# Kernel tuning notes

Measured on AMD Instinct MI355X. Metric: run time of the kernel, lower is better.

## Reference

```python
import jax, jax.numpy as jnp
import numpy as np

MAX_SAMPLES = 400  # init max_samples
EPS = 1e-9


def setup_inputs() -> dict:
    key = jax.random.key(0)
    k1, k2, k3, k4 = jax.random.split(key, 4)
    E, N, K, L = 8192, 2048, 8, 16
    # per-edge probabilities (positive, as the loss takes log of ratios)
    probas = jax.random.uniform(k1, (E,), jnp.float32, minval=1e-3, maxval=1.0)
    # soft cluster assignments: row-normalized so Bhattacharyya coeff <= 1
    c = jax.random.uniform(k2, (N, K), jnp.float32)
    clusters = c / c.sum(axis=1, keepdims=True)
    edges_nn = jax.random.randint(k3, (E, 2), 0, N)
    label_keypoints = jax.random.randint(k4, (L,), 0, N)
    return {"probas": probas, "clusters": clusters,
            "edges_nn": edges_nn, "label_keypoints": label_keypoints}


def reference(probas, clusters, edges_nn, label_keypoints):
    E = edges_nn.shape[0]
    clst = jnp.argmax(clusters, axis=1)                      # [N] hard assignment
    c0 = clst[edges_nn[:, 0]]                                # [E]
    c1 = clst[edges_nn[:, 1]]                                # [E]
    assigned = clst[label_keypoints]                         # [L] clusters at keypoints
    # edge selected if either endpoint lies in a keypoint cluster (union over labels,
    # static-shape mask form of get_edges_on_location)
    sel = jnp.any((c0[None, :] == assigned[:, None]) |
                  (c1[None, :] == assigned[:, None]), axis=0)  # [E]
    sims = c0 == c1
    pos = sel & sims                                          # positive edges
    neg = sel & ~sims                                         # negative edges
    # Bhattacharyya coefficient per edge: sum_k sqrt(p_k * q_k)
    bc = jnp.sqrt(clusters[edges_nn[:, 0]] * clusters[edges_nn[:, 1]]).sum(axis=1)  # [E]
    # pos x neg cross product, restricted to pairs sharing the anchor node edges[.,0]
    same_anchor = edges_nn[:, 0][:, None] == edges_nn[None, :, 0]   # [E,E]
    valid = pos[:, None] & neg[None, :] & same_anchor               # [E,E]
    w = 1.0 - 0.5 * (bc[:, None] + bc[None, :])                     # [E,E] sampling prob
    logw = jnp.where(valid & (w > 0),
                     jnp.log(jnp.maximum(w, EPS)), -jnp.inf)
    # multinomial-without-replacement via Gumbel top-k (deterministic key)
    u = jax.random.uniform(jax.random.key(42), (E, E), jnp.float32)
    gumbel = -jnp.log(-jnp.log(u + EPS) + EPS)
    vals, flat_idx = jax.lax.top_k((logw + gumbel).reshape(-1), MAX_SAMPLES)
    i_ = flat_idx // E                                        # positive-edge rows
    j_ = flat_idx % E                                         # negative-edge rows
    p_pos = probas[i_]
    p_neg = probas[j_]
    term = jnp.log(p_pos / (p_pos + p_neg))                   # [max_samples]
    # guard against < max_samples valid pairs (torch would just sample fewer)
    ok = jnp.isfinite(vals)
    loss = -jnp.sum(jnp.where(ok, term, 0.0)) / jnp.maximum(jnp.sum(ok), 1)
    return loss
```

## Files before the change

kernel.cpp:

```cpp
#include <hip/hip_runtime.h>
#include <stdint.h>


#define E_CONST 8192
#define N_CONST 2048
#define K_CONST 8
#define L_CONST 16
#define MAXS 400
#define EPS_F 1e-9f
#define NTHR 1024

struct Cand { float val; uint32_t pack; };

__device__ __forceinline__ uint2 threefry2x32_42(uint32_t x0, uint32_t x1) {
    const uint32_t ks0 = 0u, ks1 = 42u;
    const uint32_t ks2 = ks0 ^ ks1 ^ 0x1BD11BDAu;
    const uint32_t ks[3] = {ks0, ks1, ks2};
    const int R[2][4] = {{13, 15, 26, 6}, {17, 29, 16, 24}};
    x0 += ks0; x1 += ks1;
#pragma unroll
    for (int g = 0; g < 5; ++g) {
        const int* r = R[g & 1];
#pragma unroll
        for (int q = 0; q < 4; ++q) {
            x0 += x1;
            x1 = (x1 << r[q]) | (x1 >> (32 - r[q]));
            x1 ^= x0;
        }
        x0 += ks[(g + 1) % 3];
        x1 += ks[(g + 2) % 3] + (uint32_t)(g + 1);
    }
    return make_uint2(x0, x1);
}

__device__ __forceinline__ float gumbel_at(uint32_t idx) {
    uint2 o = threefry2x32_42(0u, idx);
    uint32_t bits = o.x ^ o.y;
    float u = __uint_as_float((bits >> 9) | 0x3F800000u) - 1.0f;
    return -logf(-logf(u + EPS_F) + EPS_F);
}

__device__ __forceinline__ uint32_t sortable_key(float f) {
    uint32_t b = __float_as_uint(f);
    return (b & 0x80000000u) ? ~b : (b | 0x80000000u);
}

__device__ __forceinline__ int argmax8(float4 a, float4 b) {
    float v[8] = {a.x, a.y, a.z, a.w, b.x, b.y, b.z, b.w};
    float best = v[0]; int bi = 0;
#pragma unroll
    for (int k = 1; k < 8; ++k)
        if (v[k] > best) { best = v[k]; bi = k; }
    return bi;
}

__global__ __launch_bounds__(128) void k_prep(
    const float* __restrict__ clusters, const int* __restrict__ edges,
    const int* __restrict__ keypts,
    float* __restrict__ bc, unsigned char* __restrict__ flags) {
    __shared__ uint32_t s_mask;
    int tid = threadIdx.x;
    if (tid == 0) s_mask = 0;
    __syncthreads();
    if (tid < L_CONST) {
        const float4* r = (const float4*)(clusters + keypts[tid] * K_CONST);
        atomicOr(&s_mask, 1u << argmax8(r[0], r[1]));
    }
    __syncthreads();
    uint32_t m = s_mask;

    int e = blockIdx.x * 128 + tid;
    const int2* ed2 = (const int2*)edges;
    const float4* c4 = (const float4*)clusters;
    int2 p = ed2[e];
    float4 a0 = c4[2 * p.x], a1 = c4[2 * p.x + 1];
    float4 b0 = c4[2 * p.y], b1 = c4[2 * p.y + 1];
    int c0 = argmax8(a0, a1);
    int c1 = argmax8(b0, b1);
    float s = sqrtf(a0.x * b0.x);
    s += sqrtf(a0.y * b0.y);
    s += sqrtf(a0.z * b0.z);
    s += sqrtf(a0.w * b0.w);
    s += sqrtf(a1.x * b1.x);
    s += sqrtf(a1.y * b1.y);
    s += sqrtf(a1.z * b1.z);
    s += sqrtf(a1.w * b1.w);
    bc[e] = s;
    unsigned char f = 0;
    if ((((m >> c0) | (m >> c1)) & 1u)) f = (c0 == c1) ? 1 : 2;
    flags[e] = f;
}

__device__ __forceinline__ void scan_inplace(int* arr, int* tmp, int* totalOut) {
    int tid = threadIdx.x;
    int lane = tid & 63, wid = tid >> 6;
    int i0 = 2 * tid, i1 = i0 + 1;
    int v0 = arr[i0], v1 = arr[i1];
    int s = v0 + v1;
    int inc = s;
#pragma unroll
    for (int off = 1; off < 64; off <<= 1) {
        int u = __shfl_up(inc, off);
        if (lane >= off) inc += u;
    }
    if (lane == 63) tmp[wid] = inc;
    __syncthreads();
    if (wid == 0) {
        int w = (lane < 16) ? tmp[lane] : 0;
        int incw = w;
#pragma unroll
        for (int off = 1; off < 16; off <<= 1) {
            int u = __shfl_up(incw, off);
            if (lane >= off) incw += u;
        }
        if (lane < 16) tmp[lane] = incw - w;
    }
    __syncthreads();
    int base = tmp[wid] + (inc - s);
    arr[i0] = base;
    arr[i1] = base + v0;
    if (tid == 1023) *totalOut = base + v0 + v1;
    __syncthreads();
}

__global__ __launch_bounds__(1024) void k_fused(
    const float* __restrict__ probas, const int* __restrict__ edges,
    const unsigned char* __restrict__ flags, const float* __restrict__ bc,
    Cand* __restrict__ cand, int pmax, float* __restrict__ out) {

    __shared__ int s_pk[N_CONST];
    __shared__ int s_q[N_CONST];
    __shared__ int s_cur[N_CONST];
    __shared__ uint16_t s_csr[E_CONST];
    __shared__ int s_tmp[16];
    __shared__ int s_hist[256];
    __shared__ float s_wsum[16];
    __shared__ int s_wcnt[16];
    __shared__ int s_totPk, s_totQ;
    __shared__ uint32_t s_prefix;
    __shared__ int s_target;

    int tid = threadIdx.x;
    s_pk[2 * tid] = 0; s_pk[2 * tid + 1] = 0;
    __syncthreads();

    const int2* ed2 = (const int2*)edges;
    uint32_t af[8];
#pragma unroll
    for (int it = 0; it < 8; ++it) {
        int e = tid + it * NTHR;
        int a = ed2[e].x;
        int f = flags[e];
        af[it] = ((uint32_t)a << 2) | (uint32_t)f;
        if (f == 1)      atomicAdd(&s_pk[a], 1);
        else if (f == 2) atomicAdd(&s_pk[a], 0x10000);
    }
    __syncthreads();

    {
        int i0 = 2 * tid, i1 = i0 + 1;
        int p0 = s_pk[i0], p1 = s_pk[i1];
        s_q[i0] = (p0 & 0xFFFF) * (p0 >> 16);
        s_q[i1] = (p1 & 0xFFFF) * (p1 >> 16);
    }
    __syncthreads();
    scan_inplace(s_pk, s_tmp, &s_totPk);
    scan_inplace(s_q, s_tmp, &s_totQ);
    s_cur[2 * tid] = s_pk[2 * tid];
    s_cur[2 * tid + 1] = s_pk[2 * tid + 1];
    __syncthreads();
    int nPosTot = s_totPk & 0xFFFF;
    int nNegTot = s_totPk >> 16;
    int P = s_totQ; if (P > pmax) P = pmax;

#pragma unroll
    for (int it = 0; it < 8; ++it) {
        int f = (int)(af[it] & 3u);
        int a = (int)(af[it] >> 2);
        int e = tid + it * NTHR;
        if (f == 1) {
            int old = atomicAdd(&s_cur[a], 1);
            s_csr[old & 0xFFFF] = (uint16_t)e;
        } else if (f == 2) {
            int old = atomicAdd(&s_cur[a], 0x10000);
            s_csr[nPosTot + (old >> 16)] = (uint16_t)e;
        }
    }
    __syncthreads();

    for (int t = tid; t < P; t += NTHR) {
        int lo = 0, hi = N_CONST - 1;
#pragma unroll
        for (int itr = 0; itr < 11; ++itr) {
            int mid = (lo + hi + 1) >> 1;
            if (s_q[mid] <= t) lo = mid; else hi = mid - 1;
        }
        int a = lo;
        int loc = t - s_q[a];
        int pk = s_pk[a];
        int pb = pk & 0xFFFF, nb = pk >> 16;
        int nextN = (a < N_CONST - 1) ? (s_pk[a + 1] >> 16) : nNegTot;
        int nn = nextN - nb;
        int ip = loc / nn;
        int jn = loc - ip * nn;
        int i = s_csr[pb + ip];
        int j = s_csr[nPosTot + nb + jn];
        float w = 1.0f - 0.5f * (bc[i] + bc[j]);
        float val = (w > 0.0f)
            ? logf(fmaxf(w, EPS_F)) + gumbel_at((uint32_t)i * E_CONST + (uint32_t)j)
            : -INFINITY;
        cand[t].val = val;
        cand[t].pack = ((uint32_t)i << 16) | (uint32_t)j;
    }
    __syncthreads();

    int M = P;
    uint32_t thr = 0;
    if (M > MAXS) {
        if (tid == 0) { s_prefix = 0; s_target = MAXS; }
        __syncthreads();
        for (int pass = 0; pass < 4; ++pass) {
            int shift = 24 - 8 * pass;
            if (tid < 256) s_hist[tid] = 0;
            __syncthreads();
            uint32_t pfx = s_prefix;
            for (int t = tid; t < M; t += NTHR) {
                uint32_t k = sortable_key(cand[t].val);
                if (pass == 0 || (k >> (shift + 8)) == pfx)
                    atomicAdd(&s_hist[(k >> shift) & 255], 1);
            }
            __syncthreads();
            if (tid < 64) {
                int h0 = s_hist[4 * tid], h1 = s_hist[4 * tid + 1];
                int h2 = s_hist[4 * tid + 2], h3 = s_hist[4 * tid + 3];
                int sincl = h0 + h1 + h2 + h3;
#pragma unroll
                for (int off = 1; off < 64; off <<= 1) {
                    int v = __shfl_down(sincl, off);
                    if (tid + off < 64) sincl += v;
                }
                int excl = __shfl_down(sincl, 1);
                if (tid == 63) excl = 0;
                int suf3 = excl + h3;
                int suf2 = suf3 + h2;
                int suf1 = suf2 + h1;
                int suf0 = suf1 + h0;
                int tgt = s_target;
                uint32_t pfxOld = s_prefix;
                if      (suf0 >= tgt && suf1 < tgt) { s_prefix = (pfxOld << 8) | (4u*tid+0); s_target = tgt - suf1; }
                else if (suf1 >= tgt && suf2 < tgt) { s_prefix = (pfxOld << 8) | (4u*tid+1); s_target = tgt - suf2; }
                else if (suf2 >= tgt && suf3 < tgt) { s_prefix = (pfxOld << 8) | (4u*tid+2); s_target = tgt - suf3; }
                else if (suf3 >= tgt && excl < tgt) { s_prefix = (pfxOld << 8) | (4u*tid+3); s_target = tgt - excl; }
            }
            __syncthreads();
        }
        thr = s_prefix;
    }

    float mysum = 0.f;
    int myc = 0;
    for (int t = tid; t < M; t += NTHR) {
        Cand c = cand[t];
        if (c.val != -INFINITY && sortable_key(c.val) >= thr) {
            int i = (int)(c.pack >> 16), j = (int)(c.pack & 0xFFFFu);
            float pi = probas[i], pj = probas[j];
            mysum += logf(pi / (pi + pj));
            myc++;
        }
    }
#pragma unroll
    for (int off = 32; off > 0; off >>= 1) {
        mysum += __shfl_down(mysum, off);
        myc   += __shfl_down(myc, off);
    }
    int wid = tid >> 6;
    if ((tid & 63) == 0) { s_wsum[wid] = mysum; s_wcnt[wid] = myc; }
    __syncthreads();
    if (tid == 0) {
        float s = 0.f; int c = 0;
        for (int w = 0; w < 16; ++w) { s += s_wsum[w]; c += s_wcnt[w]; }
        if (c < 1) c = 1;
        out[0] = -s / (float)c;
    }
}

extern "C" void kernel_launch(void* const* d_in, const int* in_sizes, int n_in,
                              void* d_out, int out_size, void* d_ws, size_t ws_size,
                              hipStream_t stream) {
    const float* probas   = (const float*)d_in[0];
    const float* clusters = (const float*)d_in[1];
    const int*   edges    = (const int*)d_in[2];
    const int*   keypts   = (const int*)d_in[3];
    float* out = (float*)d_out;

    char* ws = (char*)d_ws;
    float*         bc    = (float*)(ws);
    unsigned char* flags = (unsigned char*)(ws + 32768);
    Cand*          cand  = (Cand*)(ws + 40960);
    long long avail = (long long)ws_size - 40960;
    int pmax = (avail > 0) ? (int)(avail / 8) : 0;
    if (pmax > 65536) pmax = 65536;

    k_prep <<<64, 128, 0, stream>>>(clusters, edges, keypts, bc, flags);
    k_fused<<<1, 1024, 0, stream>>>(probas, edges, flags, bc, cand, pmax, out);
}
```

Measured before the change: 28.67 us.

## Fuse prep and selection into one cooperative kernel with register-held candidates

Merges the per-edge prep kernel and the single-block selection kernel into one cooperative launch of 64 blocks. A grid sync separates the phases, and blocks other than block 0 then exit. The first 4096 candidates are kept in registers instead of going through global memory for the histogram passes and the final accumulation, and only the excess spills to the workspace. This removes one kernel launch boundary and the repeated global reads of candidates, at the cost of cooperative-launch and grid-sync overhead and higher register pressure.

```diff
diff --git a/kernel.cpp b/kernel.cpp
--- a/kernel.cpp
+++ b/kernel.cpp
@@ -1,6 +1,9 @@
 #include <hip/hip_runtime.h>
+#include <hip/hip_cooperative_groups.h>
 #include <stdint.h>
 
+
+namespace cg = cooperative_groups;
 
 #define E_CONST 8192
 #define N_CONST 2048
@@ -9,6 +12,9 @@
 #define MAXS 400
 #define EPS_F 1e-9f
 #define NTHR 1024
+#define PREP_BLOCKS 64
+#define EDGES_PER_BLK (E_CONST / PREP_BLOCKS)
+#define RCAP 4096
 
 struct Cand { float val; uint32_t pack; };
 
@@ -52,43 +58,6 @@
     for (int k = 1; k < 8; ++k)
         if (v[k] > best) { best = v[k]; bi = k; }
     return bi;
-}
-
-__global__ __launch_bounds__(128) void k_prep(
-    const float* __restrict__ clusters, const int* __restrict__ edges,
-    const int* __restrict__ keypts,
-    float* __restrict__ bc, unsigned char* __restrict__ flags) {
-    __shared__ uint32_t s_mask;
-    int tid = threadIdx.x;
-    if (tid == 0) s_mask = 0;
-    __syncthreads();
-    if (tid < L_CONST) {
-        const float4* r = (const float4*)(clusters + keypts[tid] * K_CONST);
-        atomicOr(&s_mask, 1u << argmax8(r[0], r[1]));
-    }
-    __syncthreads();
-    uint32_t m = s_mask;
-
-    int e = blockIdx.x * 128 + tid;
-    const int2* ed2 = (const int2*)edges;
-    const float4* c4 = (const float4*)clusters;
-    int2 p = ed2[e];
-    float4 a0 = c4[2 * p.x], a1 = c4[2 * p.x + 1];
-    float4 b0 = c4[2 * p.y], b1 = c4[2 * p.y + 1];
-    int c0 = argmax8(a0, a1);
-    int c1 = argmax8(b0, b1);
-    float s = sqrtf(a0.x * b0.x);
-    s += sqrtf(a0.y * b0.y);
-    s += sqrtf(a0.z * b0.z);
-    s += sqrtf(a0.w * b0.w);
-    s += sqrtf(a1.x * b1.x);
-    s += sqrtf(a1.y * b1.y);
-    s += sqrtf(a1.z * b1.z);
-    s += sqrtf(a1.w * b1.w);
-    bc[e] = s;
-    unsigned char f = 0;
-    if ((((m >> c0) | (m >> c1)) & 1u)) f = (c0 == c1) ? 1 : 2;
-    flags[e] = f;
 }
 
 __device__ __forceinline__ void scan_inplace(int* arr, int* tmp, int* totalOut) {
@@ -123,10 +92,11 @@
     __syncthreads();
 }
 
-__global__ __launch_bounds__(1024) void k_fused(
-    const float* __restrict__ probas, const int* __restrict__ edges,
-    const unsigned char* __restrict__ flags, const float* __restrict__ bc,
-    Cand* __restrict__ cand, int pmax, float* __restrict__ out) {
+__global__ __launch_bounds__(1024) void k_all(
+    const float* __restrict__ probas, const float* __restrict__ clusters,
+    const int* __restrict__ edges, const int* __restrict__ keypts,
+    float* __restrict__ bc, unsigned char* __restrict__ flags,
+    Cand* __restrict__ spill, int pmax, float* __restrict__ out) {
 
     __shared__ int s_pk[N_CONST];
     __shared__ int s_q[N_CONST];
@@ -136,11 +106,47 @@
     __shared__ int s_hist[256];
     __shared__ float s_wsum[16];
     __shared__ int s_wcnt[16];
+    __shared__ uint32_t s_mask;
     __shared__ int s_totPk, s_totQ;
     __shared__ uint32_t s_prefix;
     __shared__ int s_target;
 
     int tid = threadIdx.x;
+
+    if (tid == 0) s_mask = 0;
+    __syncthreads();
+    if (tid < L_CONST) {
+        const float4* r = (const float4*)(clusters + keypts[tid] * K_CONST);
+        atomicOr(&s_mask, 1u << argmax8(r[0], r[1]));
+    }
+    __syncthreads();
+    uint32_t m = s_mask;
+    if (tid < EDGES_PER_BLK) {
+        int e = blockIdx.x * EDGES_PER_BLK + tid;
+        const int2* ed2 = (const int2*)edges;
+        const float4* c4 = (const float4*)clusters;
+        int2 p = ed2[e];
+        float4 a0 = c4[2 * p.x], a1 = c4[2 * p.x + 1];
+        float4 b0 = c4[2 * p.y], b1 = c4[2 * p.y + 1];
+        int c0 = argmax8(a0, a1);
+        int c1 = argmax8(b0, b1);
+        float s = sqrtf(a0.x * b0.x);
+        s += sqrtf(a0.y * b0.y);
+        s += sqrtf(a0.z * b0.z);
+        s += sqrtf(a0.w * b0.w);
+        s += sqrtf(a1.x * b1.x);
+        s += sqrtf(a1.y * b1.y);
+        s += sqrtf(a1.z * b1.z);
+        s += sqrtf(a1.w * b1.w);
+        bc[e] = s;
+        unsigned char f = 0;
+        if ((((m >> c0) | (m >> c1)) & 1u)) f = (c0 == c1) ? 1 : 2;
+        flags[e] = f;
+    }
+
+    cg::this_grid().sync();
+    if (blockIdx.x != 0) return;
+
     s_pk[2 * tid] = 0; s_pk[2 * tid + 1] = 0;
     __syncthreads();
 
@@ -188,7 +194,7 @@
     }
     __syncthreads();
 
-    for (int t = tid; t < P; t += NTHR) {
+    auto make_cand = [&](int t, float& val, uint32_t& pack) {
         int lo = 0, hi = N_CONST - 1;
 #pragma unroll
         for (int itr = 0; itr < 11; ++itr) {
@@ -206,12 +212,25 @@
         int i = s_csr[pb + ip];
         int j = s_csr[nPosTot + nb + jn];
         float w = 1.0f - 0.5f * (bc[i] + bc[j]);
-        float val = (w > 0.0f)
+        val = (w > 0.0f)
             ? logf(fmaxf(w, EPS_F)) + gumbel_at((uint32_t)i * E_CONST + (uint32_t)j)
             : -INFINITY;
-        cand[t].val = val;
-        cand[t].pack = ((uint32_t)i << 16) | (uint32_t)j;
-    }
+        pack = ((uint32_t)i << 16) | (uint32_t)j;
+    };
+
+    float vval0 = 0.f, vval1 = 0.f, vval2 = 0.f, vval3 = 0.f;
+    uint32_t vpk0 = 0, vpk1 = 0, vpk2 = 0, vpk3 = 0;
+    if (tid          < P) make_cand(tid,          vval0, vpk0);
+    if (tid + 1024   < P) make_cand(tid + 1024,   vval1, vpk1);
+    if (tid + 2048   < P) make_cand(tid + 2048,   vval2, vpk2);
+    if (tid + 3072   < P) make_cand(tid + 3072,   vval3, vpk3);
+    for (int t = tid + RCAP; t < P; t += NTHR) {
+        float v; uint32_t pk;
+        make_cand(t, v, pk);
+        spill[t - RCAP].val = v; spill[t - RCAP].pack = pk;
+    }
+    uint32_t vk0 = sortable_key(vval0), vk1 = sortable_key(vval1);
+    uint32_t vk2 = sortable_key(vval2), vk3 = sortable_key(vval3);
     __syncthreads();
 
     int M = P;
@@ -224,8 +243,12 @@
             if (tid < 256) s_hist[tid] = 0;
             __syncthreads();
             uint32_t pfx = s_prefix;
-            for (int t = tid; t < M; t += NTHR) {
-                uint32_t k = sortable_key(cand[t].val);
+            if (tid          < M && (pass == 0 || (vk0 >> (shift + 8)) == pfx)) atomicAdd(&s_hist[(vk0 >> shift) & 255], 1);
+            if (tid + 1024   < M && (pass == 0 || (vk1 >> (shift + 8)) == pfx)) atomicAdd(&s_hist[(vk1 >> shift) & 255], 1);
+            if (tid + 2048   < M && (pass == 0 || (vk2 >> (shift + 8)) == pfx)) atomicAdd(&s_hist[(vk2 >> shift) & 255], 1);
+            if (tid + 3072   < M && (pass == 0 || (vk3 >> (shift + 8)) == pfx)) atomicAdd(&s_hist[(vk3 >> shift) & 255], 1);
+            for (int t = tid + RCAP; t < M; t += NTHR) {
+                uint32_t k = sortable_key(spill[t - RCAP].val);
                 if (pass == 0 || (k >> (shift + 8)) == pfx)
                     atomicAdd(&s_hist[(k >> shift) & 255], 1);
             }
@@ -259,14 +282,21 @@
 
     float mysum = 0.f;
     int myc = 0;
-    for (int t = tid; t < M; t += NTHR) {
-        Cand c = cand[t];
-        if (c.val != -INFINITY && sortable_key(c.val) >= thr) {
-            int i = (int)(c.pack >> 16), j = (int)(c.pack & 0xFFFFu);
+    auto accum = [&](int t, float v, uint32_t k, uint32_t pk) {
+        if (t < M && v != -INFINITY && k >= thr) {
+            int i = (int)(pk >> 16), j = (int)(pk & 0xFFFFu);
             float pi = probas[i], pj = probas[j];
             mysum += logf(pi / (pi + pj));
             myc++;
         }
+    };
+    accum(tid,        vval0, vk0, vpk0);
+    accum(tid + 1024, vval1, vk1, vpk1);
+    accum(tid + 2048, vval2, vk2, vpk2);
+    accum(tid + 3072, vval3, vk3, vpk3);
+    for (int t = tid + RCAP; t < M; t += NTHR) {
+        Cand c = spill[t - RCAP];
+        accum(t, c.val, sortable_key(c.val), c.pack);
     }
 #pragma unroll
     for (int off = 32; off > 0; off >>= 1) {
@@ -296,11 +326,14 @@
     char* ws = (char*)d_ws;
     float*         bc    = (float*)(ws);
     unsigned char* flags = (unsigned char*)(ws + 32768);
-    Cand*          cand  = (Cand*)(ws + 40960);
+    Cand*          spill = (Cand*)(ws + 40960);
     long long avail = (long long)ws_size - 40960;
-    int pmax = (avail > 0) ? (int)(avail / 8) : 0;
-    if (pmax > 65536) pmax = 65536;
-
-    k_prep <<<64, 128, 0, stream>>>(clusters, edges, keypts, bc, flags);
-    k_fused<<<1, 1024, 0, stream>>>(probas, edges, flags, bc, cand, pmax, out);
-}
+    int spill_cap = (avail > 0) ? (int)(avail / 8) : 0;
+    if (spill_cap > 61440) spill_cap = 61440;
+    int pmax = RCAP + spill_cap;
+
+    void* args[] = {(void*)&probas, (void*)&clusters, (void*)&edges, (void*)&keypts,
+                    (void*)&bc, (void*)&flags, (void*)&spill, (void*)&pmax, (void*)&out};
+    hipLaunchCooperativeKernel((const void*)k_all, dim3(PREP_BLOCKS), dim3(NTHR),
+                               args, 0, stream);
+}
```

Result: slower. 49.55 us (+72.8%).
